# Kernel tuning notes

Hardware: AMD Instinct MI355X
Metric: run time of the kernel (lower is better)

The kernel has to match this reference:

```python
import jax, jax.numpy as jnp
import numpy as np

IGNORE_INDEX = -100
N, C = 2097152, 32


def setup_inputs() -> dict:
    key = jax.random.key(0)
    k1, k2, k3 = jax.random.split(key, 3)
    pred = jax.random.normal(k1, (N, C), dtype=jnp.float32)
    # neg_count (~0.95N) > pos_num * factor (~0.15N).
    r = jax.random.randint(k2, (N,), 0, 100, dtype=jnp.int32)
    cls = jax.random.randint(k3, (N,), 1, C, dtype=jnp.int32)
    label = jnp.where(r >= 95, cls, 0).astype(jnp.int32)
    return {"pred": pred, "label": label, "factor": 3}


def reference(pred, label, factor):
    n = pred.shape[0]
    is_pos = label != 0
    pos_num = jnp.sum(is_pos)
    neg_sum = pos_num * factor
    num_neg = n - pos_num

    # max non-background score per row
    pred_value = jnp.max(pred[:, 1:], axis=1)  # [N]

    # descending sort of negative-position scores (positives pushed to the end)
    neg_scores = jnp.where(is_pos, -jnp.inf, pred_value)
    sorted_desc = -jnp.sort(-neg_scores)
    idx = jnp.clip(neg_sum - 1, 0, n - 1)
    threshold = sorted_desc[idx]

    mask_thr = (pred_value >= threshold) | is_pos
    mask_all = label != -1
    mask = jnp.where(num_neg > neg_sum, mask_thr, mask_all)
    mask = jax.lax.stop_gradient(mask)  # torch computes mask on detached numpy

    masked_label = jnp.where(mask, label, IGNORE_INDEX)
    valid = masked_label != IGNORE_INDEX
    safe_label = jnp.where(valid, masked_label, 0)

    logp = jax.nn.log_softmax(pred, axis=-1)  # [N, C]
    nll = -jnp.take_along_axis(logp, safe_label[:, None], axis=1)[:, 0]  # [N]
    denom = jnp.maximum(jnp.sum(valid), 1)
    loss = jnp.sum(jnp.where(valid, nll, 0.0)) / denom.astype(pred.dtype)
    return loss
```

## Files before the change

### kernel.cpp

```cpp
#include <hip/hip_runtime.h>


typedef float f4 __attribute__((ext_vector_type(4)));

#define TILE_ROWS 256
#define ROW_F4    9

struct Ctrl {
    unsigned hist8[256];
    unsigned hist12[4096];
    unsigned bcnt[4096];
    float    bsum[4096];
    unsigned pos_num;
    unsigned cnt;
    unsigned done;
    unsigned pad;
    double   sum;
};

__global__ void init_kernel(unsigned* w, int words) {
    for (int i = threadIdx.x + blockIdx.x * blockDim.x; i < words;
         i += blockDim.x * gridDim.x)
        w[i] = 0u;
}

__device__ inline void wave_hist_add(unsigned* h, unsigned bucket) {
    unsigned long long todo = __ballot(1);
    while (todo) {
        int leader = (int)__builtin_ctzll(todo);
        unsigned b = __shfl(bucket, leader);
        unsigned long long same = __ballot(bucket == b) & todo;
        if ((int)(threadIdx.x & 63) == leader)
            atomicAdd(&h[b], (unsigned)__popcll(same));
        todo &= ~same;
    }
}

__global__ void __launch_bounds__(256)
row_kernel(const f4* __restrict__ pred4, const int* __restrict__ label,
           unsigned* __restrict__ keys, float* __restrict__ nll,
           Ctrl* __restrict__ c, int n) {
    __shared__ f4 tile[TILE_ROWS * ROW_F4];
    __shared__ unsigned h[256];
    for (int i = threadIdx.x; i < 256; i += 256) h[i] = 0u;
    __syncthreads();

    const int tid = threadIdx.x;
    int pos_local = 0;
    const int tile_stride = gridDim.x * TILE_ROWS;

    for (int tbase = blockIdx.x * TILE_ROWS; tbase < n; tbase += tile_stride) {
#pragma unroll
        for (int k = 0; k < 8; ++k) {
            int idx = (k << 8) + tid;
            f4 v = pred4[(size_t)tbase * 8 + idx];
            tile[(idx >> 3) * ROW_F4 + (idx & 7)] = v;
        }
        __syncthreads();

        int row = tbase + tid;
        float r[32];
#pragma unroll
        for (int j = 0; j < 8; ++j) {
            f4 v = tile[tid * ROW_F4 + j];
            r[4 * j + 0] = v.x; r[4 * j + 1] = v.y;
            r[4 * j + 2] = v.z; r[4 * j + 3] = v.w;
        }
        float m_nb = r[1];
#pragma unroll
        for (int j = 2; j < 32; ++j) m_nb = fmaxf(m_nb, r[j]);
        float m_all = fmaxf(m_nb, r[0]);

        float s = 0.f;
#pragma unroll
        for (int j = 0; j < 32; ++j) s += __expf(r[j] - m_all);

        int lab = label[row];
        int sl = lab; sl = sl < 0 ? 0 : sl; sl = sl > 31 ? 31 : sl;
        float xl = r[0];
#pragma unroll
        for (int j = 1; j < 32; ++j) xl = (j == sl) ? r[j] : xl;

        nll[row] = (m_all + __logf(s)) - xl;

        bool is_pos = (lab != 0);
        pos_local += is_pos ? 1 : 0;

        float ns = is_pos ? -__builtin_inff() : m_nb;
        unsigned u    = __float_as_uint(ns);
        unsigned ukey = (u & 0x80000000u) ? ~u : (u | 0x80000000u);
        unsigned dkey = ~ukey;
        keys[row] = dkey;
        wave_hist_add(h, dkey >> 24);

        __syncthreads();
    }

#pragma unroll
    for (int off = 32; off > 0; off >>= 1) pos_local += __shfl_down(pos_local, off);
    __shared__ int wsum[4];
    int wid = threadIdx.x >> 6;
    if ((threadIdx.x & 63) == 0) wsum[wid] = pos_local;
    __syncthreads();
    if (threadIdx.x == 0)
        atomicAdd(&c->pos_num, (unsigned)(wsum[0] + wsum[1] + wsum[2] + wsum[3]));

    for (int i = threadIdx.x; i < 256; i += 256)
        if (h[i]) atomicAdd(&c->hist8[i], h[i]);
}

__device__ inline void block_scan256(unsigned* s) {
    const int t = threadIdx.x;
#pragma unroll
    for (int off = 1; off < 256; off <<= 1) {
        unsigned v = (t >= off) ? s[t - off] : 0u;
        __syncthreads();
        s[t] += v;
        __syncthreads();
    }
}

__device__ inline void rank_params(const Ctrl* c, int factor, int n,
                                   unsigned& rank, bool& use_thr) {
    long long pos     = (long long)c->pos_num;
    long long neg_sum = pos * (long long)factor;
    long long num_neg = (long long)n - pos;
    long long idx     = neg_sum - 1;
    if (idx < 0) idx = 0;
    if (idx > (long long)n - 1) idx = (long long)n - 1;
    rank    = (unsigned)idx;
    use_thr = (num_neg > neg_sum);
}

__device__ inline void select_byte3(const Ctrl* c, unsigned rank, unsigned* s,
                                    unsigned* shbr, unsigned& b3, unsigned& rank1) {
    const int t = threadIdx.x;
    unsigned cnt8 = c->hist8[t];
    s[t] = cnt8;
    __syncthreads();
    block_scan256(s);
    unsigned incl = s[t], excl = incl - cnt8;
    if (cnt8 > 0u && excl <= rank && rank < incl) {
        shbr[0] = (unsigned)t;
        shbr[1] = rank - excl;
    }
    __syncthreads();
    b3 = shbr[0];
    rank1 = shbr[1];
    __syncthreads();
}

__device__ inline void select_12(const unsigned* hist, unsigned rank_in,
                                 unsigned* s, unsigned* shbr,
                                 unsigned& sub, unsigned& rank_out) {
    const int t = threadIdx.x;
    unsigned lc[16]; unsigned lsum = 0u;
#pragma unroll
    for (int i = 0; i < 16; ++i) { lc[i] = hist[t * 16 + i]; lsum += lc[i]; }
    s[t] = lsum;
    __syncthreads();
    block_scan256(s);
    unsigned incl = s[t], excl = incl - lsum;
    if (lsum > 0u && excl <= rank_in && rank_in < incl) {
        unsigned r = rank_in - excl;
#pragma unroll
        for (int i = 0; i < 16; ++i) {
            if (r < lc[i]) { shbr[0] = (unsigned)(t * 16 + i); shbr[1] = r; break; }
            r -= lc[i];
        }
    }
    __syncthreads();
    sub = shbr[0];
    rank_out = shbr[1];
    __syncthreads();
}

__global__ void __launch_bounds__(256)
hist12_kernel(const unsigned* __restrict__ keys, Ctrl* __restrict__ c,
              const int* __restrict__ factor_p, int n) {
    __shared__ unsigned s[256];
    __shared__ unsigned shbr[2];
    __shared__ unsigned h[4096];
    const int t = threadIdx.x;

    unsigned rank; bool use_thr;
    rank_params(c, factor_p[0], n, rank, use_thr);
    unsigned b3, rank1;
    select_byte3(c, rank, s, shbr, b3, rank1);

    for (int i = t; i < 4096; i += 256) h[i] = 0u;
    __syncthreads();

    const int stride = gridDim.x * blockDim.x;
    for (int i = blockIdx.x * blockDim.x + t; i < n; i += stride) {
        unsigned k = keys[i];
        if ((k >> 24) == b3) atomicAdd(&h[(k >> 12) & 0xFFFu], 1u);
    }
    __syncthreads();
    for (int i = t; i < 4096; i += 256)
        if (h[i]) atomicAdd(&c->hist12[i], h[i]);
}

__global__ void __launch_bounds__(256)
reduceF_kernel(const unsigned* __restrict__ keys, const int* __restrict__ label,
               const float* __restrict__ nll, Ctrl* __restrict__ c,
               const int* __restrict__ factor_p, int n, float* __restrict__ out) {
    __shared__ unsigned s[256];
    __shared__ unsigned shbr[2];
    __shared__ double sd[4];
    __shared__ int    si[4];
    const int t = threadIdx.x, lane = t & 63, wid = t >> 6;

    unsigned rank; bool use_thr;
    rank_params(c, factor_p[0], n, rank, use_thr);
    unsigned b3, rank1;
    select_byte3(c, rank, s, shbr, b3, rank1);
    unsigned sub, rank2;
    select_12(c->hist12, rank1, s, shbr, sub, rank2);
    const unsigned prefix20 = (b3 << 12) | sub;

    double local = 0.0;
    int cntl = 0;
    const int stride = gridDim.x * blockDim.x;
    for (int i = blockIdx.x * blockDim.x + t; i < n; i += stride) {
        int lab = label[i];
        float nl = nll[i];
        if (use_thr) {
            unsigned k = keys[i];
            unsigned top20 = k >> 12;
            if (lab != 0 || top20 < prefix20) { local += (double)nl; cntl++; }
            else if (top20 == prefix20) {
                atomicAdd(&c->bcnt[k & 0xFFFu], 1u);
                atomicAdd(&c->bsum[k & 0xFFFu], nl);
            }
        } else {
            if (lab != -1) { local += (double)nl; cntl++; }
        }
    }
#pragma unroll
    for (int off = 32; off > 0; off >>= 1) {
        local += __shfl_down(local, off);
        cntl  += __shfl_down(cntl, off);
    }
    if (lane == 0) { sd[wid] = local; si[wid] = cntl; }
    __syncthreads();
    __shared__ int s_last;
    if (t == 0) {
        atomicAdd(&c->sum, sd[0] + sd[1] + sd[2] + sd[3]);
        atomicAdd(&c->cnt, (unsigned)(si[0] + si[1] + si[2] + si[3]));
        __threadfence();
        unsigned d = atomicAdd(&c->done, 1u);
        s_last = (d == gridDim.x - 1) ? 1 : 0;
    }
    __syncthreads();
    if (!s_last) return;

    __threadfence();
    __shared__ double   fssum;
    __shared__ unsigned fscnt;
    if (t == 0) { fssum = 0.0; fscnt = 0u; }
    __syncthreads();
    if (use_thr) {
        unsigned bstar, dummy;
        select_12(c->bcnt, rank2, s, shbr, bstar, dummy);
        double fsl = 0.0; unsigned fcl = 0u;
        for (int i = t; i < 4096; i += 256)
            if ((unsigned)i <= bstar) { fcl += c->bcnt[i]; fsl += (double)c->bsum[i]; }
#pragma unroll
        for (int off = 32; off > 0; off >>= 1) {
            fsl += __shfl_down(fsl, off);
            fcl += __shfl_down(fcl, off);
        }
        if (lane == 0) { sd[wid] = fsl; si[wid] = (int)fcl; }
        __syncthreads();
        if (t == 0) {
            fssum = sd[0] + sd[1] + sd[2] + sd[3];
            fscnt = (unsigned)(si[0] + si[1] + si[2] + si[3]);
        }
        __syncthreads();
    }
    if (t == 0) {
        double sm = c->sum + fssum;
        unsigned ctn = c->cnt + fscnt;
        double denom = (ctn == 0u) ? 1.0 : (double)ctn;
        out[0] = (float)(sm / denom);
    }
}

extern "C" void kernel_launch(void* const* d_in, const int* in_sizes, int n_in,
                              void* d_out, int out_size, void* d_ws, size_t ws_size,
                              hipStream_t stream) {
    const float* pred = (const float*)d_in[0];
    const int* label  = (const int*)d_in[1];
    const int* factor = (const int*)d_in[2];
    int n = in_sizes[1];
    float* out = (float*)d_out;

    char* ws = (char*)d_ws;
    Ctrl* c = (Ctrl*)ws;
    unsigned* keys = (unsigned*)(ws + 65536);
    float* nll = (float*)(ws + 65536 + (size_t)n * 4);

    init_kernel<<<64, 256, 0, stream>>>((unsigned*)c, (int)(sizeof(Ctrl) / 4));
    row_kernel<<<2048, 256, 0, stream>>>((const f4*)pred, label, keys, nll, c, n);
    hist12_kernel<<<1024, 256, 0, stream>>>(keys, c, factor, n);
    reduceF_kernel<<<1024, 256, 0, stream>>>(keys, label, nll, c, factor, n, out);
}
```

Before: 144.6 us.

## Fuse row, histogram and reduction kernels into one persistent kernel with grid barriers

Merges the three separate kernels into one persistent kernel of 512 blocks that moves between phases through a software grid barrier built on atomic counter and generation words. This removes two kernel launch gaps and the per-kernel setup. It reuses the tile shared memory for the 12-bit histogram, skips the hist12 pass when the threshold branch is not taken, and reads the label logit directly from shared memory instead of running a select loop. In exchange, the kernel relies on all 512 blocks being resident at once to avoid deadlock, and the row phase runs with fewer blocks than before.

```diff
diff --git a/kernel.cpp b/kernel.cpp
--- a/kernel.cpp
+++ b/kernel.cpp
@@ -5,6 +5,7 @@
 
 #define TILE_ROWS 256
 #define ROW_F4    9
+#define GRID_BLKS 512
 
 struct Ctrl {
     unsigned hist8[256];
@@ -13,8 +14,8 @@
     float    bsum[4096];
     unsigned pos_num;
     unsigned cnt;
-    unsigned done;
-    unsigned pad;
+    unsigned bar_cnt;
+    unsigned bar_gen;
     double   sum;
 };
 
@@ -22,6 +23,28 @@
     for (int i = threadIdx.x + blockIdx.x * blockDim.x; i < words;
          i += blockDim.x * gridDim.x)
         w[i] = 0u;
+}
+
+__device__ inline void grid_barrier(unsigned* cnt, unsigned* gen, unsigned nb) {
+    __threadfence();
+    __syncthreads();
+    if (threadIdx.x == 0) {
+        unsigned g = __hip_atomic_load(gen, __ATOMIC_ACQUIRE,
+                                       __HIP_MEMORY_SCOPE_AGENT);
+        unsigned a = __hip_atomic_fetch_add(cnt, 1u, __ATOMIC_ACQ_REL,
+                                            __HIP_MEMORY_SCOPE_AGENT);
+        if (a == nb - 1u) {
+            __hip_atomic_store(cnt, 0u, __ATOMIC_RELAXED,
+                               __HIP_MEMORY_SCOPE_AGENT);
+            __hip_atomic_fetch_add(gen, 1u, __ATOMIC_RELEASE,
+                                   __HIP_MEMORY_SCOPE_AGENT);
+        } else {
+            while (__hip_atomic_load(gen, __ATOMIC_ACQUIRE,
+                                     __HIP_MEMORY_SCOPE_AGENT) == g)
+                __builtin_amdgcn_s_sleep(1);
+        }
+    }
+    __syncthreads();
 }
 
 __device__ inline void wave_hist_add(unsigned* h, unsigned bucket) {
@@ -34,79 +57,6 @@
             atomicAdd(&h[b], (unsigned)__popcll(same));
         todo &= ~same;
     }
-}
-
-__global__ void __launch_bounds__(256)
-row_kernel(const f4* __restrict__ pred4, const int* __restrict__ label,
-           unsigned* __restrict__ keys, float* __restrict__ nll,
-           Ctrl* __restrict__ c, int n) {
-    __shared__ f4 tile[TILE_ROWS * ROW_F4];
-    __shared__ unsigned h[256];
-    for (int i = threadIdx.x; i < 256; i += 256) h[i] = 0u;
-    __syncthreads();
-
-    const int tid = threadIdx.x;
-    int pos_local = 0;
-    const int tile_stride = gridDim.x * TILE_ROWS;
-
-    for (int tbase = blockIdx.x * TILE_ROWS; tbase < n; tbase += tile_stride) {
-#pragma unroll
-        for (int k = 0; k < 8; ++k) {
-            int idx = (k << 8) + tid;
-            f4 v = pred4[(size_t)tbase * 8 + idx];
-            tile[(idx >> 3) * ROW_F4 + (idx & 7)] = v;
-        }
-        __syncthreads();
-
-        int row = tbase + tid;
-        float r[32];
-#pragma unroll
-        for (int j = 0; j < 8; ++j) {
-            f4 v = tile[tid * ROW_F4 + j];
-            r[4 * j + 0] = v.x; r[4 * j + 1] = v.y;
-            r[4 * j + 2] = v.z; r[4 * j + 3] = v.w;
-        }
-        float m_nb = r[1];
-#pragma unroll
-        for (int j = 2; j < 32; ++j) m_nb = fmaxf(m_nb, r[j]);
-        float m_all = fmaxf(m_nb, r[0]);
-
-        float s = 0.f;
-#pragma unroll
-        for (int j = 0; j < 32; ++j) s += __expf(r[j] - m_all);
-
-        int lab = label[row];
-        int sl = lab; sl = sl < 0 ? 0 : sl; sl = sl > 31 ? 31 : sl;
-        float xl = r[0];
-#pragma unroll
-        for (int j = 1; j < 32; ++j) xl = (j == sl) ? r[j] : xl;
-
-        nll[row] = (m_all + __logf(s)) - xl;
-
-        bool is_pos = (lab != 0);
-        pos_local += is_pos ? 1 : 0;
-
-        float ns = is_pos ? -__builtin_inff() : m_nb;
-        unsigned u    = __float_as_uint(ns);
-        unsigned ukey = (u & 0x80000000u) ? ~u : (u | 0x80000000u);
-        unsigned dkey = ~ukey;
-        keys[row] = dkey;
-        wave_hist_add(h, dkey >> 24);
-
-        __syncthreads();
-    }
-
-#pragma unroll
-    for (int off = 32; off > 0; off >>= 1) pos_local += __shfl_down(pos_local, off);
-    __shared__ int wsum[4];
-    int wid = threadIdx.x >> 6;
-    if ((threadIdx.x & 63) == 0) wsum[wid] = pos_local;
-    __syncthreads();
-    if (threadIdx.x == 0)
-        atomicAdd(&c->pos_num, (unsigned)(wsum[0] + wsum[1] + wsum[2] + wsum[3]));
-
-    for (int i = threadIdx.x; i < 256; i += 256)
-        if (h[i]) atomicAdd(&c->hist8[i], h[i]);
 }
 
 __device__ inline void block_scan256(unsigned* s) {
@@ -176,52 +126,107 @@
 }
 
 __global__ void __launch_bounds__(256)
-hist12_kernel(const unsigned* __restrict__ keys, Ctrl* __restrict__ c,
-              const int* __restrict__ factor_p, int n) {
-    __shared__ unsigned s[256];
-    __shared__ unsigned shbr[2];
-    __shared__ unsigned h[4096];
-    const int t = threadIdx.x;
-
-    unsigned rank; bool use_thr;
-    rank_params(c, factor_p[0], n, rank, use_thr);
-    unsigned b3, rank1;
-    select_byte3(c, rank, s, shbr, b3, rank1);
-
-    for (int i = t; i < 4096; i += 256) h[i] = 0u;
-    __syncthreads();
-
-    const int stride = gridDim.x * blockDim.x;
-    for (int i = blockIdx.x * blockDim.x + t; i < n; i += stride) {
-        unsigned k = keys[i];
-        if ((k >> 24) == b3) atomicAdd(&h[(k >> 12) & 0xFFFu], 1u);
-    }
-    __syncthreads();
-    for (int i = t; i < 4096; i += 256)
-        if (h[i]) atomicAdd(&c->hist12[i], h[i]);
-}
-
-__global__ void __launch_bounds__(256)
-reduceF_kernel(const unsigned* __restrict__ keys, const int* __restrict__ label,
-               const float* __restrict__ nll, Ctrl* __restrict__ c,
-               const int* __restrict__ factor_p, int n, float* __restrict__ out) {
+fused_kernel(const f4* __restrict__ pred4, const int* __restrict__ label,
+             const int* __restrict__ factor_p, unsigned* __restrict__ keys,
+             float* __restrict__ nll, Ctrl* __restrict__ c,
+             float* __restrict__ out, int n) {
+    __shared__ f4 tile[TILE_ROWS * ROW_F4];
+    __shared__ unsigned h[256];
     __shared__ unsigned s[256];
     __shared__ unsigned shbr[2];
     __shared__ double sd[4];
     __shared__ int    si[4];
     const int t = threadIdx.x, lane = t & 63, wid = t >> 6;
-
+    const unsigned nb = gridDim.x;
+
+    h[t] = 0u;
+    __syncthreads();
+    int pos_local = 0;
+    const int tile_stride = gridDim.x * TILE_ROWS;
+    for (int tbase = blockIdx.x * TILE_ROWS; tbase < n; tbase += tile_stride) {
+#pragma unroll
+        for (int k = 0; k < 8; ++k) {
+            int idx = (k << 8) + t;
+            if (tbase + (idx >> 3) < n)
+                tile[(idx >> 3) * ROW_F4 + (idx & 7)] =
+                    pred4[(size_t)tbase * 8 + idx];
+        }
+        __syncthreads();
+
+        int row = tbase + t;
+        if (row < n) {
+            float r[32];
+#pragma unroll
+            for (int j = 0; j < 8; ++j) {
+                f4 v = tile[t * ROW_F4 + j];
+                r[4 * j + 0] = v.x; r[4 * j + 1] = v.y;
+                r[4 * j + 2] = v.z; r[4 * j + 3] = v.w;
+            }
+            float m_nb = r[1];
+#pragma unroll
+            for (int j = 2; j < 32; ++j) m_nb = fmaxf(m_nb, r[j]);
+            float m_all = fmaxf(m_nb, r[0]);
+
+            float sum = 0.f;
+#pragma unroll
+            for (int j = 0; j < 32; ++j) sum += __expf(r[j] - m_all);
+
+            int lab = label[row];
+            int sl = lab; sl = sl < 0 ? 0 : sl; sl = sl > 31 ? 31 : sl;
+            float xl = ((const float*)tile)[t * (ROW_F4 * 4) + sl];
+
+            nll[row] = (m_all + __logf(sum)) - xl;
+
+            bool is_pos = (lab != 0);
+            pos_local += is_pos ? 1 : 0;
+
+            float ns = is_pos ? -__builtin_inff() : m_nb;
+            unsigned u    = __float_as_uint(ns);
+            unsigned ukey = (u & 0x80000000u) ? ~u : (u | 0x80000000u);
+            unsigned dkey = ~ukey;
+            keys[row] = dkey;
+            wave_hist_add(h, dkey >> 24);
+        }
+        __syncthreads();
+    }
+#pragma unroll
+    for (int off = 32; off > 0; off >>= 1) pos_local += __shfl_down(pos_local, off);
+    if (lane == 0) si[wid] = pos_local;
+    __syncthreads();
+    if (t == 0)
+        atomicAdd(&c->pos_num, (unsigned)(si[0] + si[1] + si[2] + si[3]));
+    if (h[t]) atomicAdd(&c->hist8[t], h[t]);
+
+    grid_barrier(&c->bar_cnt, &c->bar_gen, nb);
+
+    const int factor = factor_p[0];
     unsigned rank; bool use_thr;
-    rank_params(c, factor_p[0], n, rank, use_thr);
+    rank_params(c, factor, n, rank, use_thr);
     unsigned b3, rank1;
     select_byte3(c, rank, s, shbr, b3, rank1);
-    unsigned sub, rank2;
-    select_12(c->hist12, rank1, s, shbr, sub, rank2);
+
+    unsigned* h12 = (unsigned*)tile;
+    const int stride = gridDim.x * blockDim.x;
+    if (use_thr) {
+        for (int i = t; i < 4096; i += 256) h12[i] = 0u;
+        __syncthreads();
+        for (int i = blockIdx.x * blockDim.x + t; i < n; i += stride) {
+            unsigned k = keys[i];
+            if ((k >> 24) == b3) atomicAdd(&h12[(k >> 12) & 0xFFFu], 1u);
+        }
+        __syncthreads();
+        for (int i = t; i < 4096; i += 256)
+            if (h12[i]) atomicAdd(&c->hist12[i], h12[i]);
+    }
+
+    grid_barrier(&c->bar_cnt, &c->bar_gen, nb);
+
+    unsigned sub = 0u, rank2 = 0u;
+    if (use_thr) select_12(c->hist12, rank1, s, shbr, sub, rank2);
     const unsigned prefix20 = (b3 << 12) | sub;
 
     double local = 0.0;
     int cntl = 0;
-    const int stride = gridDim.x * blockDim.x;
     for (int i = blockIdx.x * blockDim.x + t; i < n; i += stride) {
         int lab = label[i];
         float nl = nll[i];
@@ -244,18 +249,14 @@
     }
     if (lane == 0) { sd[wid] = local; si[wid] = cntl; }
     __syncthreads();
-    __shared__ int s_last;
     if (t == 0) {
         atomicAdd(&c->sum, sd[0] + sd[1] + sd[2] + sd[3]);
         atomicAdd(&c->cnt, (unsigned)(si[0] + si[1] + si[2] + si[3]));
-        __threadfence();
-        unsigned d = atomicAdd(&c->done, 1u);
-        s_last = (d == gridDim.x - 1) ? 1 : 0;
-    }
-    __syncthreads();
-    if (!s_last) return;
-
-    __threadfence();
+    }
+
+    grid_barrier(&c->bar_cnt, &c->bar_gen, nb);
+
+    if (blockIdx.x != 0) return;
     __shared__ double   fssum;
     __shared__ unsigned fscnt;
     if (t == 0) { fssum = 0.0; fscnt = 0u; }
@@ -302,7 +303,6 @@
     float* nll = (float*)(ws + 65536 + (size_t)n * 4);
 
     init_kernel<<<64, 256, 0, stream>>>((unsigned*)c, (int)(sizeof(Ctrl) / 4));
-    row_kernel<<<2048, 256, 0, stream>>>((const f4*)pred, label, keys, nll, c, n);
-    hist12_kernel<<<1024, 256, 0, stream>>>(keys, c, factor, n);
-    reduceF_kernel<<<1024, 256, 0, stream>>>(keys, label, nll, c, factor, n, out);
-}
+    fused_kernel<<<GRID_BLKS, 256, 0, stream>>>((const f4*)pred, label, factor,
+                                                keys, nll, c, out, n);
+}
```

Measured after the change: 419.7 us. 190% more time.

## Double-buffer row tiles via direct global-to-LDS loads and drop label reads in reduce

Applied to the files above, without the earlier changes.

The row kernel now stages each 256-row tile straight into LDS with global_load_lds, using a swizzled layout and two buffers so the next tile streams in while the current one is computed. The grid shrinks to 512 blocks so each block loops over more tiles. Max and exp-sum reductions are split into four independent accumulators. The reduce kernel identifies positives from the sentinel key instead of rereading labels, and skips the second-level select when no threshold is needed. Risks are lower occupancy from the larger LDS footprint and extra waitcnt and barrier stalls.

```diff
diff --git a/kernel.cpp b/kernel.cpp
--- a/kernel.cpp
+++ b/kernel.cpp
@@ -4,7 +4,7 @@
 typedef float f4 __attribute__((ext_vector_type(4)));
 
 #define TILE_ROWS 256
-#define ROW_F4    9
+#define ROW_GRID  512
 
 struct Ctrl {
     unsigned hist8[256];
@@ -40,73 +40,111 @@
 row_kernel(const f4* __restrict__ pred4, const int* __restrict__ label,
            unsigned* __restrict__ keys, float* __restrict__ nll,
            Ctrl* __restrict__ c, int n) {
-    __shared__ f4 tile[TILE_ROWS * ROW_F4];
+    __shared__ f4 buf[2][TILE_ROWS * 8];
     __shared__ unsigned h[256];
-    for (int i = threadIdx.x; i < 256; i += 256) h[i] = 0u;
-    __syncthreads();
-
-    const int tid = threadIdx.x;
+    __shared__ int wsum[4];
+    const int t  = threadIdx.x;
+    const int t7 = t & 7;
+    h[t] = 0u;
+    __syncthreads();
+
+    const int srow = t >> 3;
+    const int gcol = t7 ^ (srow & 7);
+    const int tile_stride = gridDim.x * TILE_ROWS;
+
+    auto stage = [&](int bi, int tb) {
+#pragma unroll
+        for (int k = 0; k < 8; ++k) {
+            const f4* g = pred4 + (((size_t)(tb + k * 32 + srow)) << 3) + gcol;
+            f4* l = &buf[bi][k * 256 + (t & ~63)];
+            __builtin_amdgcn_global_load_lds(
+                (const __attribute__((address_space(1))) unsigned*)g,
+                (__attribute__((address_space(3))) unsigned*)l, 16, 0, 0);
+        }
+    };
+
     int pos_local = 0;
-    const int tile_stride = gridDim.x * TILE_ROWS;
-
-    for (int tbase = blockIdx.x * TILE_ROWS; tbase < n; tbase += tile_stride) {
-#pragma unroll
-        for (int k = 0; k < 8; ++k) {
-            int idx = (k << 8) + tid;
-            f4 v = pred4[(size_t)tbase * 8 + idx];
-            tile[(idx >> 3) * ROW_F4 + (idx & 7)] = v;
-        }
-        __syncthreads();
-
-        int row = tbase + tid;
+    int tbase = blockIdx.x * TILE_ROWS;
+    if (tbase + TILE_ROWS <= n) stage(0, tbase);
+    asm volatile("s_waitcnt vmcnt(0)" ::: "memory");
+    __syncthreads();
+
+    int cur = 0;
+    for (; tbase < n; tbase += tile_stride) {
+        int nbase = tbase + tile_stride;
+        if (nbase + TILE_ROWS <= n) stage(cur ^ 1, nbase);
+
+        int row = tbase + t;
         float r[32];
-#pragma unroll
-        for (int j = 0; j < 8; ++j) {
-            f4 v = tile[tid * ROW_F4 + j];
-            r[4 * j + 0] = v.x; r[4 * j + 1] = v.y;
-            r[4 * j + 2] = v.z; r[4 * j + 3] = v.w;
-        }
-        float m_nb = r[1];
-#pragma unroll
-        for (int j = 2; j < 32; ++j) m_nb = fmaxf(m_nb, r[j]);
-        float m_all = fmaxf(m_nb, r[0]);
-
-        float s = 0.f;
-#pragma unroll
-        for (int j = 0; j < 32; ++j) s += __expf(r[j] - m_all);
-
-        int lab = label[row];
-        int sl = lab; sl = sl < 0 ? 0 : sl; sl = sl > 31 ? 31 : sl;
-        float xl = r[0];
-#pragma unroll
-        for (int j = 1; j < 32; ++j) xl = (j == sl) ? r[j] : xl;
-
-        nll[row] = (m_all + __logf(s)) - xl;
-
-        bool is_pos = (lab != 0);
-        pos_local += is_pos ? 1 : 0;
-
-        float ns = is_pos ? -__builtin_inff() : m_nb;
-        unsigned u    = __float_as_uint(ns);
-        unsigned ukey = (u & 0x80000000u) ? ~u : (u | 0x80000000u);
-        unsigned dkey = ~ukey;
-        keys[row] = dkey;
-        wave_hist_add(h, dkey >> 24);
-
-        __syncthreads();
+        bool full = (tbase + TILE_ROWS <= n);
+        if (full) {
+            const f4* bc = buf[cur];
+#pragma unroll
+            for (int j = 0; j < 8; ++j) {
+                f4 v = bc[t * 8 + (j ^ t7)];
+                r[4*j+0] = v.x; r[4*j+1] = v.y; r[4*j+2] = v.z; r[4*j+3] = v.w;
+            }
+        } else if (row < n) {
+            const f4* p = pred4 + (size_t)row * 8;
+#pragma unroll
+            for (int j = 0; j < 8; ++j) {
+                f4 v = p[j];
+                r[4*j+0] = v.x; r[4*j+1] = v.y; r[4*j+2] = v.z; r[4*j+3] = v.w;
+            }
+        }
+
+        if (row < n) {
+            float m0 = r[1], m1 = r[2], m2 = r[3], m3 = r[4];
+#pragma unroll
+            for (int j = 5; j <= 28; j += 4) {
+                m0 = fmaxf(m0, r[j]);     m1 = fmaxf(m1, r[j+1]);
+                m2 = fmaxf(m2, r[j+2]);   m3 = fmaxf(m3, r[j+3]);
+            }
+            m0 = fmaxf(m0, r[29]); m1 = fmaxf(m1, r[30]); m2 = fmaxf(m2, r[31]);
+            float m_nb  = fmaxf(fmaxf(m0, m1), fmaxf(m2, m3));
+            float m_all = fmaxf(m_nb, r[0]);
+
+            float s0 = 0.f, s1 = 0.f, s2 = 0.f, s3 = 0.f;
+#pragma unroll
+            for (int j = 0; j < 32; j += 4) {
+                s0 += __expf(r[j]   - m_all);  s1 += __expf(r[j+1] - m_all);
+                s2 += __expf(r[j+2] - m_all);  s3 += __expf(r[j+3] - m_all);
+            }
+            float ssum = (s0 + s1) + (s2 + s3);
+
+            int lab = label[row];
+            int sl = lab; sl = sl < 0 ? 0 : sl; sl = sl > 31 ? 31 : sl;
+            float xl;
+            if (full)
+                xl = ((const float*)buf[cur])[(t*8 + ((sl>>2) ^ t7))*4 + (sl&3)];
+            else
+                xl = r[sl];
+
+            nll[row] = (m_all + __logf(ssum)) - xl;
+
+            bool is_pos = (lab != 0);
+            pos_local += is_pos ? 1 : 0;
+            float ns = is_pos ? -__builtin_inff() : m_nb;
+            unsigned u    = __float_as_uint(ns);
+            unsigned ukey = (u & 0x80000000u) ? ~u : (u | 0x80000000u);
+            unsigned dkey = ~ukey;
+            keys[row] = dkey;
+            wave_hist_add(h, dkey >> 24);
+        }
+
+        asm volatile("s_waitcnt vmcnt(0)" ::: "memory");
+        __syncthreads();
+        cur ^= 1;
     }
 
 #pragma unroll
     for (int off = 32; off > 0; off >>= 1) pos_local += __shfl_down(pos_local, off);
-    __shared__ int wsum[4];
-    int wid = threadIdx.x >> 6;
-    if ((threadIdx.x & 63) == 0) wsum[wid] = pos_local;
-    __syncthreads();
-    if (threadIdx.x == 0)
+    int wid = t >> 6;
+    if ((t & 63) == 0) wsum[wid] = pos_local;
+    __syncthreads();
+    if (t == 0)
         atomicAdd(&c->pos_num, (unsigned)(wsum[0] + wsum[1] + wsum[2] + wsum[3]));
-
-    for (int i = threadIdx.x; i < 256; i += 256)
-        if (h[i]) atomicAdd(&c->hist8[i], h[i]);
+    if (h[t]) atomicAdd(&c->hist8[t], h[t]);
 }
 
 __device__ inline void block_scan256(unsigned* s) {
@@ -215,26 +253,27 @@
     rank_params(c, factor_p[0], n, rank, use_thr);
     unsigned b3, rank1;
     select_byte3(c, rank, s, shbr, b3, rank1);
-    unsigned sub, rank2;
-    select_12(c->hist12, rank1, s, shbr, sub, rank2);
+    unsigned sub = 0u, rank2 = 0u;
+    if (use_thr) select_12(c->hist12, rank1, s, shbr, sub, rank2);
     const unsigned prefix20 = (b3 << 12) | sub;
 
     double local = 0.0;
     int cntl = 0;
     const int stride = gridDim.x * blockDim.x;
-    for (int i = blockIdx.x * blockDim.x + t; i < n; i += stride) {
-        int lab = label[i];
-        float nl = nll[i];
-        if (use_thr) {
+    if (use_thr) {
+        for (int i = blockIdx.x * blockDim.x + t; i < n; i += stride) {
             unsigned k = keys[i];
+            float nl = nll[i];
             unsigned top20 = k >> 12;
-            if (lab != 0 || top20 < prefix20) { local += (double)nl; cntl++; }
+            if (k == 0xFF800000u || top20 < prefix20) { local += (double)nl; cntl++; }
             else if (top20 == prefix20) {
                 atomicAdd(&c->bcnt[k & 0xFFFu], 1u);
                 atomicAdd(&c->bsum[k & 0xFFFu], nl);
             }
-        } else {
-            if (lab != -1) { local += (double)nl; cntl++; }
+        }
+    } else {
+        for (int i = blockIdx.x * blockDim.x + t; i < n; i += stride) {
+            if (label[i] != -1) { local += (double)nll[i]; cntl++; }
         }
     }
 #pragma unroll
@@ -302,7 +341,7 @@
     float* nll = (float*)(ws + 65536 + (size_t)n * 4);
 
     init_kernel<<<64, 256, 0, stream>>>((unsigned*)c, (int)(sizeof(Ctrl) / 4));
-    row_kernel<<<2048, 256, 0, stream>>>((const f4*)pred, label, keys, nll, c, n);
+    row_kernel<<<ROW_GRID, 256, 0, stream>>>((const f4*)pred, label, keys, nll, c, n);
     hist12_kernel<<<1024, 256, 0, stream>>>(keys, c, factor, n);
     reduceF_kernel<<<1024, 256, 0, stream>>>(keys, label, nll, c, factor, n, out);
 }
```

Result: slower. 212.8 us (+47.2%).
